# Kernel tuning notes

Hardware: AMD Instinct MI355X
Metric: run time of the kernel (lower is better)

## Reference

```python
import jax, jax.numpy as jnp
import numpy as np

N_NODES = 20000
N_REL = 200
DIM = 128
N_EDGES = 200000
N_TIMES = 8


def setup_inputs() -> dict:
    key = jax.random.key(0)
    ks = jax.random.split(key, 12)
    s = 1.0 / np.sqrt(DIM)
    return {
        "edge_index": jax.random.randint(ks[0], (2, N_EDGES), 0, N_NODES),
        "edge_type": jax.random.randint(ks[1], (N_EDGES,), 0, N_REL),
        "edge_time": jax.random.randint(ks[2], (N_EDGES,), 0, N_TIMES),
        "edge_weight": jax.random.uniform(ks[3], (N_EDGES,), dtype=jnp.float32),
        "node_emb": jax.random.normal(ks[4], (N_NODES, DIM), dtype=jnp.float32),
        "rel_emb": jax.random.normal(ks[5], (N_REL, DIM), dtype=jnp.float32),
        "W_enc": jax.random.normal(ks[6], (DIM, DIM), dtype=jnp.float32) * s,
        "Wz": jax.random.normal(ks[7], (DIM, DIM), dtype=jnp.float32) * s,
        "Uz": jax.random.normal(ks[8], (DIM, DIM), dtype=jnp.float32) * s,
        "Wh": jax.random.normal(ks[9], (DIM, DIM), dtype=jnp.float32) * s,
        "Uh": jax.random.normal(ks[10], (DIM, DIM), dtype=jnp.float32) * s,
        "bz": jnp.zeros((DIM,), dtype=jnp.float32),
        "bh": jnp.zeros((DIM,), dtype=jnp.float32),
        "num_times": N_TIMES,
    }


def reference(edge_index, edge_type, edge_time, edge_weight,
              node_emb, rel_emb, W_enc, Wz, Uz, Wh, Uh, bz, bh, num_times):
    # TemporalEncoder.forward: loop over sorted unique timestamps; per-step
    # masked-edge GNN encode (R-GCN lite) then gated SSM cell; state detached.
    src, dst = edge_index[0], edge_index[1]
    rel_e = rel_emb[edge_type]          # [E, D] gather (constant across steps)
    src_e = node_emb[src]               # [E, D]
    n_nodes = node_emb.shape[0]

    def step(state, t):
        m = (edge_time == t).astype(edge_weight.dtype)       # [E]
        msg = src_e * rel_e * (edge_weight * m)[:, None]     # [E, D]
        agg = jax.ops.segment_sum(msg, dst, num_segments=n_nodes)  # [N, D]
        h = jnp.tanh(agg @ W_enc)                            # base_encoder output
        z = jax.nn.sigmoid(h @ Wz + state @ Uz + bz)
        cand = jnp.tanh(h @ Wh + state @ Uh + bh)
        new_state = (1.0 - z) * state + z * cand             # ssm.cell
        return jax.lax.stop_gradient(new_state), new_state   # state.detach()

    state0 = jnp.zeros_like(node_emb)
    _, outs = jax.lax.scan(step, state0, jnp.arange(num_times))
    return outs[-1]  # last_out, shape [N, D]
```

## Files before the change

kernel.cpp:

```cpp
#include <hip/hip_runtime.h>

#define N_NODES 20000
#define N_EDGES 200000
#define DIM 128
#define T_STEPS 8
#define N_TILES (N_NODES / 16)
#define SCAN_N (N_NODES + 1)
#define SCAN_BLKS ((SCAN_N + 1023) / 1024)

typedef short short8 __attribute__((ext_vector_type(8)));
typedef float f32x4 __attribute__((ext_vector_type(4)));

static __device__ __forceinline__ unsigned short f2bf(float f) {
  union { float f; unsigned u; } v; v.f = f;
  unsigned r = v.u + 0x7fffu + ((v.u >> 16) & 1u);
  return (unsigned short)(r >> 16);
}
static __device__ __forceinline__ float fast_tanh(float x) {
  float e = __expf(2.f * x);
  return 1.f - 2.f / (e + 1.f);
}
static __device__ __forceinline__ float fast_sig(float x) {
  return 1.f / (1.f + __expf(-x));
}

__global__ void repack5(const float* __restrict__ w0,
                        const float* __restrict__ w1,
                        const float* __restrict__ w2,
                        const float* __restrict__ w3,
                        const float* __restrict__ w4,
                        unsigned short* __restrict__ pack) {
  int i = blockIdx.x * blockDim.x + threadIdx.x;
  if (i >= 5 * 16384) return;
  int m = i >> 14, r = i & 16383;
  int j = r & 7, lane = (r >> 3) & 63, ks = (r >> 9) & 3, nt = (r >> 11) & 7;
  int n = nt * 16 + (lane & 15);
  int k = ks * 32 + (lane >> 4) * 8 + j;
  const float* w = (m == 0) ? w0 : (m == 1) ? w1 : (m == 2) ? w2
                 : (m == 3) ? w3 : w4;
  pack[i] = f2bf(w[k * DIM + n]);
}

__global__ void hist_k(const int* __restrict__ dst, int* __restrict__ counts) {
  int i = blockIdx.x * blockDim.x + threadIdx.x;
  if (i >= N_EDGES) return;
  atomicAdd(&counts[dst[i]], 1);
}

__global__ void scan1_k(const int* __restrict__ counts,
                        int* __restrict__ base, int* __restrict__ bsum) {
  __shared__ int ls[256];
  int tid = threadIdx.x;
  int i0 = blockIdx.x * 1024 + tid * 4;
  int v[4], ts = 0;
#pragma unroll
  for (int r = 0; r < 4; r++) {
    v[r] = (i0 + r < SCAN_N) ? counts[i0 + r] : 0;
    ts += v[r];
  }
  ls[tid] = ts; __syncthreads();
#pragma unroll
  for (int off = 1; off < 256; off <<= 1) {
    int x = (tid >= off) ? ls[tid - off] : 0;
    __syncthreads(); ls[tid] += x; __syncthreads();
  }
  int run = ls[tid] - ts;
  if (tid == 255) bsum[blockIdx.x] = ls[255];
#pragma unroll
  for (int r = 0; r < 4; r++) {
    if (i0 + r < SCAN_N) base[i0 + r] = run;
    run += v[r];
  }
}

__global__ void scan2_k(int* __restrict__ bsum) {
  __shared__ int ls[256];
  int tid = threadIdx.x;
  int v = (tid < SCAN_BLKS) ? bsum[tid] : 0;
  ls[tid] = v; __syncthreads();
#pragma unroll
  for (int off = 1; off < 256; off <<= 1) {
    int x = (tid >= off) ? ls[tid - off] : 0;
    __syncthreads(); ls[tid] += x; __syncthreads();
  }
  if (tid < SCAN_BLKS) bsum[tid] = ls[tid] - v;
}

__global__ void scan3_k(int* __restrict__ base, const int* __restrict__ bsum) {
  int i = blockIdx.x * blockDim.x + threadIdx.x;
  if (i < SCAN_N) base[i] += bsum[i >> 10];
}

__global__ void fill_k(const int* __restrict__ src, const int* __restrict__ dst,
                       const int* __restrict__ etype, const int* __restrict__ etime,
                       const float* __restrict__ ew,
                       const int* __restrict__ base, int* __restrict__ cursor,
                       unsigned* __restrict__ epack, float* __restrict__ sw) {
  int i = blockIdx.x * blockDim.x + threadIdx.x;
  if (i >= N_EDGES) return;
  int d = dst[i];
  int pos = base[d] + atomicAdd(&cursor[d], 1);
  epack[pos] = (unsigned)src[i] | ((unsigned)etype[i] << 15) | ((unsigned)etime[i] << 23);
  sw[pos] = ew[i];
}

__global__ void gather_k(const int* __restrict__ base,
                         const unsigned* __restrict__ epack,
                         const float* __restrict__ sw,
                         const float* __restrict__ nemb,
                         const float* __restrict__ remb,
                         unsigned short* __restrict__ aggb) {
  int lane = threadIdx.x & 63;
  int node = (blockIdx.x * blockDim.x + threadIdx.x) >> 6;
  int s0 = base[node], s1 = base[node + 1];
  float ax[T_STEPS], ay[T_STEPS];
#pragma unroll
  for (int tt = 0; tt < T_STEPS; tt++) { ax[tt] = 0.f; ay[tt] = 0.f; }
  for (int i = s0; i < s1; i++) {
    unsigned u = epack[i];
    float w = sw[i];
    int s = u & 0x7fff, rt = (u >> 15) & 0xff, t = u >> 23;
    float2 sv = ((const float2*)(nemb + (size_t)s * DIM))[lane];
    float2 rv = ((const float2*)(remb + (size_t)rt * DIM))[lane];
    float m0 = sv.x * rv.x * w;
    float m1 = sv.y * rv.y * w;
#pragma unroll
    for (int tt = 0; tt < T_STEPS; tt++) {
      ax[tt] += (t == tt) ? m0 : 0.f;
      ay[tt] += (t == tt) ? m1 : 0.f;
    }
  }
#pragma unroll
  for (int tt = 0; tt < T_STEPS; tt++) {
    ushort2 o; o.x = f2bf(ax[tt]); o.y = f2bf(ay[tt]);
    ((ushort2*)(aggb + ((size_t)tt * N_NODES + node) * DIM))[lane] = o;
  }
}

__launch_bounds__(512)
__global__ void fused_recur(const unsigned short* __restrict__ aggb,
                            const unsigned short* __restrict__ pack,
                            const float* __restrict__ bz,
                            const float* __restrict__ bh,
                            float* __restrict__ out) {
  __shared__ unsigned short Hb[2][16 * 136];
  __shared__ unsigned short Sb[2][16 * 136];
  int lane = threadIdx.x & 63;
  int nt = threadIdx.x >> 6;
  int tile = blockIdx.x;
  int q = lane >> 4, l15 = lane & 15;
  int row0 = tile * 16;

  short8 wenc[4], wz[4], uz[4], wh[4], uh[4];
#pragma unroll
  for (int ks = 0; ks < 4; ks++) {
    int fo = ((nt * 4 + ks) * 64 + lane) * 8;
    wenc[ks] = *(const short8*)(pack + 16384 * 0 + fo);
    wz[ks]   = *(const short8*)(pack + 16384 * 1 + fo);
    uz[ks]   = *(const short8*)(pack + 16384 * 2 + fo);
    wh[ks]   = *(const short8*)(pack + 16384 * 3 + fo);
    uh[ks]   = *(const short8*)(pack + 16384 * 4 + fo);
  }
  float bzv = bz[nt * 16 + l15];
  float bhv = bh[nt * 16 + l15];

  f32x4 stC = (f32x4){0.f, 0.f, 0.f, 0.f};

  for (int t = 0; t < T_STEPS; t++) {
    f32x4 acch = (f32x4){0.f, 0.f, 0.f, 0.f};
#pragma unroll
    for (int ks = 0; ks < 4; ks++) {
      short8 aA = *(const short8*)(aggb +
          ((size_t)t * N_NODES + row0 + l15) * DIM + ks * 32 + q * 8);
      acch = __builtin_amdgcn_mfma_f32_16x16x32_bf16(aA, wenc[ks], acch, 0, 0, 0);
    }
    unsigned short* hB = Hb[t & 1];
    unsigned short* sB = Sb[t & 1];
#pragma unroll
    for (int r = 0; r < 4; r++) {
      hB[(q * 4 + r) * 136 + nt * 16 + l15] = f2bf(fast_tanh(acch[r]));
      sB[(q * 4 + r) * 136 + nt * 16 + l15] = f2bf(stC[r]);
    }
    __syncthreads();

    short8 hA[4], sA[4];
#pragma unroll
    for (int ks = 0; ks < 4; ks++) {
      hA[ks] = *(const short8*)&hB[l15 * 136 + ks * 32 + q * 8];
      sA[ks] = *(const short8*)&sB[l15 * 136 + ks * 32 + q * 8];
    }

    f32x4 accz = (f32x4){bzv, bzv, bzv, bzv};
    f32x4 accc = (f32x4){bhv, bhv, bhv, bhv};
#pragma unroll
    for (int ks = 0; ks < 4; ks++) {
      accz = __builtin_amdgcn_mfma_f32_16x16x32_bf16(hA[ks], wz[ks], accz, 0, 0, 0);
      accz = __builtin_amdgcn_mfma_f32_16x16x32_bf16(sA[ks], uz[ks], accz, 0, 0, 0);
      accc = __builtin_amdgcn_mfma_f32_16x16x32_bf16(hA[ks], wh[ks], accc, 0, 0, 0);
      accc = __builtin_amdgcn_mfma_f32_16x16x32_bf16(sA[ks], uh[ks], accc, 0, 0, 0);
    }
#pragma unroll
    for (int r = 0; r < 4; r++) {
      float z = fast_sig(accz[r]);
      float c = fast_tanh(accc[r]);
      stC[r] = (1.f - z) * stC[r] + z * c;
    }
  }

#pragma unroll
  for (int r = 0; r < 4; r++)
    out[(size_t)(row0 + q * 4 + r) * DIM + nt * 16 + l15] = stC[r];
}

extern "C" void kernel_launch(void* const* d_in, const int* in_sizes, int n_in,
                              void* d_out, int out_size, void* d_ws, size_t ws_size,
                              hipStream_t stream) {
  const int* eidx  = (const int*)d_in[0];
  const int* src   = eidx;
  const int* dst   = eidx + N_EDGES;
  const int* etype = (const int*)d_in[1];
  const int* etime = (const int*)d_in[2];
  const float* ew   = (const float*)d_in[3];
  const float* nemb = (const float*)d_in[4];
  const float* remb = (const float*)d_in[5];
  const float* Wenc = (const float*)d_in[6];
  const float* Wz   = (const float*)d_in[7];
  const float* Uz   = (const float*)d_in[8];
  const float* Wh   = (const float*)d_in[9];
  const float* Uh   = (const float*)d_in[10];
  const float* bz   = (const float*)d_in[11];
  const float* bh   = (const float*)d_in[12];

  unsigned short* aggb = (unsigned short*)d_ws;
  int* counts = (int*)(aggb + (size_t)T_STEPS * N_NODES * DIM);
  int* cursor = counts + SCAN_N;
  int* bsum   = cursor + N_NODES;
  int* base   = bsum + 64;
  unsigned* epack = (unsigned*)(base + SCAN_N);
  float* sw   = (float*)(epack + N_EDGES);
  unsigned short* pack = (unsigned short*)(sw + N_EDGES);
  float* outp = (float*)d_out;

  hipMemsetAsync(counts, 0, (size_t)(SCAN_N + N_NODES) * sizeof(int), stream);
  repack5<<<(5 * 16384 + 255) / 256, 256, 0, stream>>>(Wenc, Wz, Uz, Wh, Uh, pack);
  hist_k<<<(N_EDGES + 255) / 256, 256, 0, stream>>>(dst, counts);
  scan1_k<<<SCAN_BLKS, 256, 0, stream>>>(counts, base, bsum);
  scan2_k<<<1, 256, 0, stream>>>(bsum);
  scan3_k<<<(SCAN_N + 255) / 256, 256, 0, stream>>>(base, bsum);
  fill_k<<<(N_EDGES + 255) / 256, 256, 0, stream>>>(src, dst, etype, etime, ew,
                                                    base, cursor, epack, sw);
  gather_k<<<N_NODES / 4, 256, 0, stream>>>(base, epack, sw, nemb, remb, aggb);
  fused_recur<<<N_TILES, 512, 0, stream>>>(aggb, pack, bz, bh, outp);
}
```

Baseline: 222.8 us.

## Sort edges by (node,time) key and hoist encoder GEMM out of recurrence

The CSR build now keys edges by destination node and timestep, so the gather kernel walks each time bucket with one scalar accumulator pair instead of 8 predicated accumulators per edge. The recurrence kernel precomputes all tanh(agg@W_enc) tiles before the state loop and holds them packed in registers, which frees the W_enc registers during the loop and takes the global loads off the serial chain. It also uses the packed bf16 convert instruction and adds a launch bounds occupancy hint. In exchange, the scan covers eight times more keys, and the larger register footprint may limit occupancy. scan2 assumes SCAN_BLKS fits in 256 threads.

```diff
diff --git a/kernel.cpp b/kernel.cpp
--- a/kernel.cpp
+++ b/kernel.cpp
@@ -1,11 +1,13 @@
 #include <hip/hip_runtime.h>
 
 #define N_NODES 20000
+#define N_REL 200
 #define N_EDGES 200000
 #define DIM 128
 #define T_STEPS 8
 #define N_TILES (N_NODES / 16)
-#define SCAN_N (N_NODES + 1)
+#define KEYS (N_NODES * T_STEPS)
+#define SCAN_N (KEYS + 1)
 #define SCAN_BLKS ((SCAN_N + 1023) / 1024)
 
 typedef short short8 __attribute__((ext_vector_type(8)));
@@ -15,6 +17,11 @@
   union { float f; unsigned u; } v; v.f = f;
   unsigned r = v.u + 0x7fffu + ((v.u >> 16) & 1u);
   return (unsigned short)(r >> 16);
+}
+static __device__ __forceinline__ unsigned cvt_pk_bf16(float lo, float hi) {
+  unsigned r;
+  asm("v_cvt_pk_bf16_f32 %0, %1, %2" : "=v"(r) : "v"(lo), "v"(hi));
+  return r;
 }
 static __device__ __forceinline__ float fast_tanh(float x) {
   float e = __expf(2.f * x);
@@ -41,10 +48,11 @@
   pack[i] = f2bf(w[k * DIM + n]);
 }
 
-__global__ void hist_k(const int* __restrict__ dst, int* __restrict__ counts) {
+__global__ void hist_k(const int* __restrict__ dst, const int* __restrict__ etime,
+                       int* __restrict__ counts) {
   int i = blockIdx.x * blockDim.x + threadIdx.x;
   if (i >= N_EDGES) return;
-  atomicAdd(&counts[dst[i]], 1);
+  atomicAdd(&counts[dst[i] * T_STEPS + etime[i]], 1);
 }
 
 __global__ void scan1_k(const int* __restrict__ counts,
@@ -98,9 +106,9 @@
                        unsigned* __restrict__ epack, float* __restrict__ sw) {
   int i = blockIdx.x * blockDim.x + threadIdx.x;
   if (i >= N_EDGES) return;
-  int d = dst[i];
-  int pos = base[d] + atomicAdd(&cursor[d], 1);
-  epack[pos] = (unsigned)src[i] | ((unsigned)etype[i] << 15) | ((unsigned)etime[i] << 23);
+  int key = dst[i] * T_STEPS + etime[i];
+  int pos = base[key] + atomicAdd(&cursor[key], 1);
+  epack[pos] = (unsigned)src[i] | ((unsigned)etype[i] << 15);
   sw[pos] = ew[i];
 }
 
@@ -112,32 +120,27 @@
                          unsigned short* __restrict__ aggb) {
   int lane = threadIdx.x & 63;
   int node = (blockIdx.x * blockDim.x + threadIdx.x) >> 6;
-  int s0 = base[node], s1 = base[node + 1];
-  float ax[T_STEPS], ay[T_STEPS];
-#pragma unroll
-  for (int tt = 0; tt < T_STEPS; tt++) { ax[tt] = 0.f; ay[tt] = 0.f; }
-  for (int i = s0; i < s1; i++) {
-    unsigned u = epack[i];
-    float w = sw[i];
-    int s = u & 0x7fff, rt = (u >> 15) & 0xff, t = u >> 23;
-    float2 sv = ((const float2*)(nemb + (size_t)s * DIM))[lane];
-    float2 rv = ((const float2*)(remb + (size_t)rt * DIM))[lane];
-    float m0 = sv.x * rv.x * w;
-    float m1 = sv.y * rv.y * w;
-#pragma unroll
-    for (int tt = 0; tt < T_STEPS; tt++) {
-      ax[tt] += (t == tt) ? m0 : 0.f;
-      ay[tt] += (t == tt) ? m1 : 0.f;
-    }
-  }
+  const int* b = base + node * T_STEPS;
+  int i = b[0];
 #pragma unroll
   for (int tt = 0; tt < T_STEPS; tt++) {
-    ushort2 o; o.x = f2bf(ax[tt]); o.y = f2bf(ay[tt]);
-    ((ushort2*)(aggb + ((size_t)tt * N_NODES + node) * DIM))[lane] = o;
-  }
-}
-
-__launch_bounds__(512)
+    int e1 = b[tt + 1];
+    float ax = 0.f, ay = 0.f;
+    for (; i < e1; i++) {
+      unsigned u = epack[i];
+      float w = sw[i];
+      int s = u & 0x7fff, rt = u >> 15;
+      float2 sv = ((const float2*)(nemb + (size_t)s * DIM))[lane];
+      float2 rv = ((const float2*)(remb + (size_t)rt * DIM))[lane];
+      ax += sv.x * rv.x * w;
+      ay += sv.y * rv.y * w;
+    }
+    ((unsigned*)(aggb + ((size_t)tt * N_NODES + node) * DIM))[lane] =
+        cvt_pk_bf16(ax, ay);
+  }
+}
+
+__launch_bounds__(512, 4)
 __global__ void fused_recur(const unsigned short* __restrict__ aggb,
                             const unsigned short* __restrict__ pack,
                             const float* __restrict__ bz,
@@ -151,59 +154,73 @@
   int q = lane >> 4, l15 = lane & 15;
   int row0 = tile * 16;
 
-  short8 wenc[4], wz[4], uz[4], wh[4], uh[4];
+  unsigned hpk[T_STEPS][2];
+  {
+    short8 wenc[4];
+#pragma unroll
+    for (int ks = 0; ks < 4; ks++)
+      wenc[ks] = *(const short8*)(pack + ((nt * 4 + ks) * 64 + lane) * 8);
+#pragma unroll
+    for (int t = 0; t < T_STEPS; t++) {
+      f32x4 acch = (f32x4){0.f, 0.f, 0.f, 0.f};
+#pragma unroll
+      for (int ks = 0; ks < 4; ks++) {
+        short8 aA = *(const short8*)(aggb +
+            ((size_t)t * N_NODES + row0 + l15) * DIM + ks * 32 + q * 8);
+        acch = __builtin_amdgcn_mfma_f32_16x16x32_bf16(aA, wenc[ks], acch, 0, 0, 0);
+      }
+      hpk[t][0] = cvt_pk_bf16(fast_tanh(acch[0]), fast_tanh(acch[1]));
+      hpk[t][1] = cvt_pk_bf16(fast_tanh(acch[2]), fast_tanh(acch[3]));
+    }
+  }
+
+  short8 wz[4], uz[4], wh[4], uh[4];
 #pragma unroll
   for (int ks = 0; ks < 4; ks++) {
     int fo = ((nt * 4 + ks) * 64 + lane) * 8;
-    wenc[ks] = *(const short8*)(pack + 16384 * 0 + fo);
-    wz[ks]   = *(const short8*)(pack + 16384 * 1 + fo);
-    uz[ks]   = *(const short8*)(pack + 16384 * 2 + fo);
-    wh[ks]   = *(const short8*)(pack + 16384 * 3 + fo);
-    uh[ks]   = *(const short8*)(pack + 16384 * 4 + fo);
+    wz[ks] = *(const short8*)(pack + 16384 * 1 + fo);
+    uz[ks] = *(const short8*)(pack + 16384 * 2 + fo);
+    wh[ks] = *(const short8*)(pack + 16384 * 3 + fo);
+    uh[ks] = *(const short8*)(pack + 16384 * 4 + fo);
   }
   float bzv = bz[nt * 16 + l15];
   float bhv = bh[nt * 16 + l15];
 
   f32x4 stC = (f32x4){0.f, 0.f, 0.f, 0.f};
-
+  int c = nt * 16 + l15;
+
+#pragma unroll
   for (int t = 0; t < T_STEPS; t++) {
-    f32x4 acch = (f32x4){0.f, 0.f, 0.f, 0.f};
-#pragma unroll
-    for (int ks = 0; ks < 4; ks++) {
-      short8 aA = *(const short8*)(aggb +
-          ((size_t)t * N_NODES + row0 + l15) * DIM + ks * 32 + q * 8);
-      acch = __builtin_amdgcn_mfma_f32_16x16x32_bf16(aA, wenc[ks], acch, 0, 0, 0);
-    }
     unsigned short* hB = Hb[t & 1];
     unsigned short* sB = Sb[t & 1];
-#pragma unroll
-    for (int r = 0; r < 4; r++) {
-      hB[(q * 4 + r) * 136 + nt * 16 + l15] = f2bf(fast_tanh(acch[r]));
-      sB[(q * 4 + r) * 136 + nt * 16 + l15] = f2bf(stC[r]);
-    }
+    unsigned s01 = cvt_pk_bf16(stC[0], stC[1]);
+    unsigned s23 = cvt_pk_bf16(stC[2], stC[3]);
+    hB[(q * 4 + 0) * 136 + c] = (unsigned short)hpk[t][0];
+    hB[(q * 4 + 1) * 136 + c] = (unsigned short)(hpk[t][0] >> 16);
+    hB[(q * 4 + 2) * 136 + c] = (unsigned short)hpk[t][1];
+    hB[(q * 4 + 3) * 136 + c] = (unsigned short)(hpk[t][1] >> 16);
+    sB[(q * 4 + 0) * 136 + c] = (unsigned short)s01;
+    sB[(q * 4 + 1) * 136 + c] = (unsigned short)(s01 >> 16);
+    sB[(q * 4 + 2) * 136 + c] = (unsigned short)s23;
+    sB[(q * 4 + 3) * 136 + c] = (unsigned short)(s23 >> 16);
     __syncthreads();
-
-    short8 hA[4], sA[4];
-#pragma unroll
-    for (int ks = 0; ks < 4; ks++) {
-      hA[ks] = *(const short8*)&hB[l15 * 136 + ks * 32 + q * 8];
-      sA[ks] = *(const short8*)&sB[l15 * 136 + ks * 32 + q * 8];
-    }
 
     f32x4 accz = (f32x4){bzv, bzv, bzv, bzv};
     f32x4 accc = (f32x4){bhv, bhv, bhv, bhv};
 #pragma unroll
     for (int ks = 0; ks < 4; ks++) {
-      accz = __builtin_amdgcn_mfma_f32_16x16x32_bf16(hA[ks], wz[ks], accz, 0, 0, 0);
-      accz = __builtin_amdgcn_mfma_f32_16x16x32_bf16(sA[ks], uz[ks], accz, 0, 0, 0);
-      accc = __builtin_amdgcn_mfma_f32_16x16x32_bf16(hA[ks], wh[ks], accc, 0, 0, 0);
-      accc = __builtin_amdgcn_mfma_f32_16x16x32_bf16(sA[ks], uh[ks], accc, 0, 0, 0);
+      short8 hA = *(const short8*)&hB[l15 * 136 + ks * 32 + q * 8];
+      short8 sA = *(const short8*)&sB[l15 * 136 + ks * 32 + q * 8];
+      accz = __builtin_amdgcn_mfma_f32_16x16x32_bf16(hA, wz[ks], accz, 0, 0, 0);
+      accz = __builtin_amdgcn_mfma_f32_16x16x32_bf16(sA, uz[ks], accz, 0, 0, 0);
+      accc = __builtin_amdgcn_mfma_f32_16x16x32_bf16(hA, wh[ks], accc, 0, 0, 0);
+      accc = __builtin_amdgcn_mfma_f32_16x16x32_bf16(sA, uh[ks], accc, 0, 0, 0);
     }
 #pragma unroll
     for (int r = 0; r < 4; r++) {
       float z = fast_sig(accz[r]);
-      float c = fast_tanh(accc[r]);
-      stC[r] = (1.f - z) * stC[r] + z * c;
+      float cc = fast_tanh(accc[r]);
+      stC[r] = (1.f - z) * stC[r] + z * cc;
     }
   }
 
@@ -234,16 +251,16 @@
   unsigned short* aggb = (unsigned short*)d_ws;
   int* counts = (int*)(aggb + (size_t)T_STEPS * N_NODES * DIM);
   int* cursor = counts + SCAN_N;
-  int* bsum   = cursor + N_NODES;
-  int* base   = bsum + 64;
+  int* bsum   = cursor + KEYS;
+  int* base   = bsum + 256;
   unsigned* epack = (unsigned*)(base + SCAN_N);
   float* sw   = (float*)(epack + N_EDGES);
   unsigned short* pack = (unsigned short*)(sw + N_EDGES);
   float* outp = (float*)d_out;
 
-  hipMemsetAsync(counts, 0, (size_t)(SCAN_N + N_NODES) * sizeof(int), stream);
+  hipMemsetAsync(counts, 0, (size_t)(SCAN_N + KEYS) * sizeof(int), stream);
   repack5<<<(5 * 16384 + 255) / 256, 256, 0, stream>>>(Wenc, Wz, Uz, Wh, Uh, pack);
-  hist_k<<<(N_EDGES + 255) / 256, 256, 0, stream>>>(dst, counts);
+  hist_k<<<(N_EDGES + 255) / 256, 256, 0, stream>>>(dst, etime, counts);
   scan1_k<<<SCAN_BLKS, 256, 0, stream>>>(counts, base, bsum);
   scan2_k<<<1, 256, 0, stream>>>(bsum);
   scan3_k<<<(SCAN_N + 255) / 256, 256, 0, stream>>>(base, bsum);
```

After: 226.1 us. About the same (+1.5%).
